# Performance work log

Hardware: AMD Instinct MI355X
Metric: run time of the kernel (lower is better)

Reference implementation:

```python
import jax, jax.numpy as jnp
import numpy as np

N_NODES = 100000
N_EDGES = 1600000
HIDDEN = 128
TOKENS = 50000
NUM_GRAPHS = 128


def _gru_cell(inp, h, Wih, Whh, bih, bhh):
    # PyTorch GRUCell math. Wih, Whh: [3H, H]; bih, bhh: [3H]
    gi = inp @ Wih.T + bih
    gh = h @ Whh.T + bhh
    i_r, i_z, i_n = jnp.split(gi, 3, axis=-1)
    h_r, h_z, h_n = jnp.split(gh, 3, axis=-1)
    r = jax.nn.sigmoid(i_r + h_r)
    z = jax.nn.sigmoid(i_z + h_z)
    n = jnp.tanh(i_n + r * h_n)
    return (1.0 - z) * n + z * h


def setup_inputs() -> dict:
    key = jax.random.key(0)
    ks = jax.random.split(key, 16)
    x = jax.random.randint(ks[0], (N_NODES,), 0, TOKENS)
    edge_index = jax.random.randint(ks[1], (2, N_EDGES), 0, N_NODES)
    batch = jnp.sort(jax.random.randint(ks[2], (N_NODES,), 0, NUM_GRAPHS))
    s = 0.05
    emb = jax.random.normal(ks[3], (TOKENS, HIDDEN), jnp.float32) * s
    Wih0 = jax.random.normal(ks[4], (3 * HIDDEN, HIDDEN), jnp.float32) * s
    Whh0 = jax.random.normal(ks[5], (3 * HIDDEN, HIDDEN), jnp.float32) * s
    bih0 = jnp.zeros((3 * HIDDEN,), jnp.float32)
    bhh0 = jnp.zeros((3 * HIDDEN,), jnp.float32)
    Wih1 = jax.random.normal(ks[6], (3 * HIDDEN, HIDDEN), jnp.float32) * s
    Whh1 = jax.random.normal(ks[7], (3 * HIDDEN, HIDDEN), jnp.float32) * s
    bih1 = jnp.zeros((3 * HIDDEN,), jnp.float32)
    bhh1 = jnp.zeros((3 * HIDDEN,), jnp.float32)
    dense_W = jax.random.normal(ks[8], (HIDDEN, HIDDEN), jnp.float32) * s
    dense_b = jnp.zeros((HIDDEN,), jnp.float32)
    clf_W = jax.random.normal(ks[9], (1, HIDDEN), jnp.float32) * s
    clf_b = jnp.zeros((1,), jnp.float32)
    return {"x": x, "edge_index": edge_index, "batch": batch, "emb": emb,
            "Wih0": Wih0, "Whh0": Whh0, "bih0": bih0, "bhh0": bhh0,
            "Wih1": Wih1, "Whh1": Whh1, "bih1": bih1, "bhh1": bhh1,
            "dense_W": dense_W, "dense_b": dense_b, "clf_W": clf_W, "clf_b": clf_b}


def reference(x, edge_index, batch, emb, Wih0, Whh0, bih0, bhh0,
              Wih1, Whh1, bih1, bhh1, dense_W, dense_b, clf_W, clf_b):
    src, dst = edge_index[0], edge_index[1]
    h = emb[x]  # [N, H]
    for (Wih, Whh, bih, bhh) in ((Wih0, Whh0, bih0, bhh0), (Wih1, Whh1, bih1, bhh1)):
        # gather source features, scatter-add into targets (aggr='add')
        agg = jax.ops.segment_sum(h[src], dst, num_segments=N_NODES)
        h = _gru_cell(agg, h, Wih, Whh, bih, bhh)
    # dropout is identity in eval mode
    h = h @ dense_W.T + dense_b
    g = jax.ops.segment_max(h, batch, num_segments=NUM_GRAPHS)  # global_max_pool
    out = jax.nn.sigmoid(g @ clf_W.T + clf_b)
    return out.squeeze(-1)  # [NUM_GRAPHS]
```

## Files before the change

### kernel.cpp

```cpp
#include <hip/hip_runtime.h>
#include <hip/hip_bf16.h>
#include <math.h>

#define HID 128
#define POOL_P 4
#define NPART 8
#define NCHUNK 32
#define MAXBIN 12544
#define FSLAB 520

typedef __attribute__((ext_vector_type(8))) short bf16x8;
typedef __attribute__((ext_vector_type(4))) float f32x4;
typedef __attribute__((ext_vector_type(4))) int int4v;

__device__ __forceinline__ short f2bf(float f) {
    unsigned int u = __float_as_uint(f);
    u += 0x7FFF + ((u >> 16) & 1);
    return (short)(u >> 16);
}
__device__ __forceinline__ float bf2f(short s) {
    return __uint_as_float(((unsigned int)(unsigned short)s) << 16);
}

__device__ __forceinline__ float fexp2(float x) {
    float r;
    asm("v_exp_f32 %0, %1\n\ts_nop 0" : "=v"(r) : "v"(x));
    return r;
}
__device__ __forceinline__ float frcp(float x) {
    float r;
    asm("v_rcp_f32 %0, %1\n\ts_nop 0" : "=v"(r) : "v"(x));
    return r;
}
__device__ __forceinline__ float fsigmoid(float x) {
    return frcp(1.f + fexp2(-1.44269504f * x));
}
__device__ __forceinline__ float ftanh(float x) {
    return 1.f - 2.f * frcp(1.f + fexp2(2.88539008f * x));
}

__global__ __launch_bounds__(1024) void radix_embed_k(const int* __restrict__ x,
                                                      const float* __restrict__ emb,
                                                      short* __restrict__ h, int nnodes,
                                                      const int* __restrict__ dst,
                                                      int* __restrict__ ghist,
                                                      int nedges, int NPB, int ECH) {
    __shared__ int lh[MAXBIN];
    const int t = threadIdx.x;
    if ((int)blockIdx.x < NPART * NCHUNK) {
        const int part = blockIdx.x & (NPART - 1);
        const int chunk = blockIdx.x >> 3;
        const int lo = part * NPB;
        const int hi = min(lo + NPB, nnodes);
        const int nb = hi - lo;
        for (int b = t; b < nb; b += 1024) lh[b] = 0;
        __syncthreads();
        const int e0 = chunk * ECH;
        const int e1 = min(nedges, e0 + ECH);
        for (int base = e0; base < e1; base += 4096) {
            int e = base + (t << 2);
            if (e + 4 <= e1) {
                int4v d4 = *(const int4v*)(dst + e);
                #pragma unroll
                for (int k = 0; k < 4; ++k) {
                    int d = d4[k];
                    if (d >= lo && d < hi) atomicAdd(&lh[d - lo], 1);
                }
            } else {
                for (int k = 0; k < 4 && e + k < e1; ++k) {
                    int d = dst[e + k];
                    if (d >= lo && d < hi) atomicAdd(&lh[d - lo], 1);
                }
            }
        }
        __syncthreads();
        int* out = ghist + (size_t)blockIdx.x * NPB;
        for (int b = t; b < nb; b += 1024) out[b] = lh[b];
    } else {
        int bi = blockIdx.x - NPART * NCHUNK;
        int tid = bi * 1024 + t;
        int node = tid >> 4;
        int c8 = tid & 15;
        if (node >= nnodes) return;
        int tok = x[node];
        float4 f0 = ((const float4*)emb)[(size_t)tok * 32 + c8 * 2];
        float4 f1 = ((const float4*)emb)[(size_t)tok * 32 + c8 * 2 + 1];
        bf16x8 o;
        o[0] = f2bf(f0.x); o[1] = f2bf(f0.y); o[2] = f2bf(f0.z); o[3] = f2bf(f0.w);
        o[4] = f2bf(f1.x); o[5] = f2bf(f1.y); o[6] = f2bf(f1.z); o[7] = f2bf(f1.w);
        *(bf16x8*)(h + (size_t)node * HID + c8 * 8) = o;
    }
}

__global__ __launch_bounds__(256) void chunksum_k(int* __restrict__ ghist,
                                                  int* __restrict__ degsum,
                                                  int nnodes, int NPB) {
    int node = blockIdx.x * 256 + threadIdx.x;
    if (node >= nnodes) return;
    int part = node / NPB;
    int bin = node - part * NPB;
    int running = 0;
    #pragma unroll 4
    for (int c = 0; c < NCHUNK; ++c) {
        size_t idx = (size_t)(part + NPART * c) * NPB + bin;
        int v = ghist[idx];
        ghist[idx] = running;
        running += v;
    }
    degsum[node] = running;
}

__global__ __launch_bounds__(1024) void scan_k(const int* __restrict__ deg,
                                               int* __restrict__ rowstart,
                                               int n, int* bsum, int* bflag, int nblocks) {
    __shared__ int wsum[16];
    __shared__ int prefix_s, total_s;
    const int b = blockIdx.x;
    const int t = threadIdx.x, lane = t & 63, w = t >> 6;
    const int i4 = b * 4096 + t * 4;
    int4 v = make_int4(0, 0, 0, 0);
    if (i4 + 3 < n) v = *(const int4*)(deg + i4);
    else if (i4 < n) {
        v.x = deg[i4];
        if (i4 + 1 < n) v.y = deg[i4 + 1];
        if (i4 + 2 < n) v.z = deg[i4 + 2];
    }
    int s1 = v.x + v.y, s2 = s1 + v.z, s3 = s2 + v.w;
    int sum = s3;
    #pragma unroll
    for (int off = 1; off < 64; off <<= 1) {
        int o = __shfl_up(sum, off, 64);
        if (lane >= off) sum += o;
    }
    if (lane == 63) wsum[w] = sum;
    __syncthreads();
    if (t == 0) {
        int run = 0;
        #pragma unroll
        for (int k = 0; k < 16; ++k) { int xx = wsum[k]; wsum[k] = run; run += xx; }
        total_s = run;
        atomicExch(&bsum[b], run);
        __threadfence();
        atomicExch(&bflag[b], 1);
    }
    __syncthreads();
    if (w == 0) {
        int p = 0;
        if (lane < b) {
            while (atomicAdd(&bflag[lane], 0) == 0) {}
            p = atomicAdd(&bsum[lane], 0);
        }
        #pragma unroll
        for (int off = 32; off >= 1; off >>= 1) p += __shfl_down(p, off, 64);
        if (lane == 0) prefix_s = p;
    }
    __syncthreads();
    const int excl = (sum - s3) + wsum[w] + prefix_s;
    if (i4 + 3 < n) {
        *(int4*)(rowstart + i4) = make_int4(excl, excl + v.x, excl + s1, excl + s2);
    } else if (i4 < n) {
        rowstart[i4] = excl;
        if (i4 + 1 < n) rowstart[i4 + 1] = excl + v.x;
        if (i4 + 2 < n) rowstart[i4 + 2] = excl + s1;
    }
    if (b == nblocks - 1 && t == 1023) rowstart[n] = prefix_s + total_s;
}

__global__ __launch_bounds__(1024) void fill2_k(const int* __restrict__ src,
                                                const int* __restrict__ dst,
                                                const int* __restrict__ rowstart,
                                                const int* __restrict__ ghist,
                                                int* __restrict__ sorted_src,
                                                int nedges, int nnodes, int NPB, int ECH) {
    __shared__ int cur[MAXBIN];
    const int t = threadIdx.x;
    const int part = blockIdx.x & (NPART - 1);
    const int chunk = blockIdx.x >> 3;
    const int lo = part * NPB;
    const int hi = min(lo + NPB, nnodes);
    const int nb = hi - lo;
    const int* base = ghist + (size_t)blockIdx.x * NPB;
    for (int b = t; b < nb; b += 1024)
        cur[b] = rowstart[lo + b] + base[b];
    __syncthreads();
    const int e0 = chunk * ECH;
    const int e1 = min(nedges, e0 + ECH);
    for (int bb = e0; bb < e1; bb += 4096) {
        int e = bb + (t << 2);
        if (e + 4 <= e1) {
            int4v d4 = *(const int4v*)(dst + e);
            #pragma unroll
            for (int k = 0; k < 4; ++k) {
                int d = d4[k];
                if (d >= lo && d < hi) {
                    int s = src[e + k];
                    int pos = atomicAdd(&cur[d - lo], 1);
                    sorted_src[pos] = s;
                }
            }
        } else {
            for (int k = 0; k < 4 && e + k < e1; ++k) {
                int d = dst[e + k];
                if (d >= lo && d < hi) {
                    int s = src[e + k];
                    int pos = atomicAdd(&cur[d - lo], 1);
                    sorted_src[pos] = s;
                }
            }
        }
    }
}

__global__ __launch_bounds__(256) void gather_k(const int* __restrict__ rowstart,
                                                const int* __restrict__ sorted_src,
                                                const short* __restrict__ h,
                                                short* __restrict__ agg, int nnodes) {
    int tid = blockIdx.x * 256 + threadIdx.x;
    int node = tid >> 4;
    int l = tid & 15;
    if (node >= nnodes) return;
    int beg = rowstart[node];
    int end = rowstart[node + 1];
    const bf16x8* hr = (const bf16x8*)h;
    float a[8];
    #pragma unroll
    for (int i = 0; i < 8; ++i) a[i] = 0.f;
    int e = beg;
    for (; e + 4 <= end; e += 4) {
        int s0 = sorted_src[e];
        int s1 = sorted_src[e + 1];
        int s2 = sorted_src[e + 2];
        int s3 = sorted_src[e + 3];
        bf16x8 v0 = hr[(size_t)s0 * 16 + l];
        bf16x8 v1 = hr[(size_t)s1 * 16 + l];
        bf16x8 v2 = hr[(size_t)s2 * 16 + l];
        bf16x8 v3 = hr[(size_t)s3 * 16 + l];
        #pragma unroll
        for (int i = 0; i < 8; ++i) a[i] += bf2f(v0[i]);
        #pragma unroll
        for (int i = 0; i < 8; ++i) a[i] += bf2f(v1[i]);
        #pragma unroll
        for (int i = 0; i < 8; ++i) a[i] += bf2f(v2[i]);
        #pragma unroll
        for (int i = 0; i < 8; ++i) a[i] += bf2f(v3[i]);
    }
    for (; e < end; ++e) {
        bf16x8 v0 = hr[(size_t)sorted_src[e] * 16 + l];
        #pragma unroll
        for (int i = 0; i < 8; ++i) a[i] += bf2f(v0[i]);
    }
    bf16x8 o;
    #pragma unroll
    for (int i = 0; i < 8; ++i) o[i] = f2bf(a[i]);
    *(bf16x8*)(agg + (size_t)node * HID + l * 8) = o;
}

__global__ __launch_bounds__(256) void pack_all_k(const float* __restrict__ Wih0,
                                                  const float* __restrict__ Whh0,
                                                  const float* __restrict__ Wih1,
                                                  const float* __restrict__ Whh1,
                                                  const float* __restrict__ dW,
                                                  short* __restrict__ P0,
                                                  short* __restrict__ P1,
                                                  short* __restrict__ Pd) {
    int b = blockIdx.x;
    const float* WA; const float* WB; short* P; int ntilesA; int tile;
    if (b < 48)      { WA = Wih0; WB = Whh0; P = P0; ntilesA = 24; tile = b; }
    else if (b < 96) { WA = Wih1; WB = Whh1; P = P1; ntilesA = 24; tile = b - 48; }
    else             { WA = dW;   WB = dW;   P = Pd; ntilesA = 8;  tile = b - 96; }
    const int t = threadIdx.x;
    const int lane = t & 63, k0 = t >> 6;
    const float* W;
    int row;
    if (tile < ntilesA) { W = WA; row = tile * 16 + (lane & 15); }
    else                { W = WB; row = (tile - ntilesA) * 16 + (lane & 15); }
    const int k = k0 * 32 + (lane >> 4) * 8;
    const float4 f0 = *(const float4*)(W + row * HID + k);
    const float4 f1 = *(const float4*)(W + row * HID + k + 4);
    short4 o0 = make_short4(f2bf(f0.x), f2bf(f0.y), f2bf(f0.z), f2bf(f0.w));
    short4 o1 = make_short4(f2bf(f1.x), f2bf(f1.y), f2bf(f1.z), f2bf(f1.w));
    short* dstp = P + ((size_t)(tile * 4 + k0) * 64 + lane) * 8;
    *(short4*)(dstp) = o0;
    *(short4*)(dstp + 4) = o1;
}


__global__ __launch_bounds__(256) void gru_mfma_k(const short* __restrict__ agg,
                                                  const short* __restrict__ hin,
                                                  short* __restrict__ hout,
                                                  const short* __restrict__ P,
                                                  const float* __restrict__ bih,
                                                  const float* __restrict__ bhh,
                                                  int nnodes) {
    __shared__ short As[4 * FSLAB];
    __shared__ short Hs[4 * FSLAB];
    const int t = threadIdx.x;
    const int mbase = blockIdx.x * 16;
    {
        int row = t >> 4, c8 = t & 15;
        int node = mbase + row;
        bf16x8 a = (bf16x8){0,0,0,0,0,0,0,0};
        bf16x8 hh = (bf16x8){0,0,0,0,0,0,0,0};
        if (node < nnodes) {
            a  = *(const bf16x8*)(agg + (size_t)node * HID + c8 * 8);
            hh = *(const bf16x8*)(hin + (size_t)node * HID + c8 * 8);
        }
        int off = (c8 >> 2) * FSLAB + ((c8 & 3) * 16 + row) * 8;
        *(bf16x8*)&As[off] = a;
        *(bf16x8*)&Hs[off] = hh;
    }
    __syncthreads();

    const int w = t >> 6, lane = t & 63;
    const int ml = lane & 15, kq = lane >> 4;
    const int j0 = w * 32;

    f32x4 acc[12];
    #pragma unroll
    for (int i = 0; i < 12; ++i) acc[i] = (f32x4){0.f, 0.f, 0.f, 0.f};

    const short* Pb = P + (size_t)lane * 8;

    #pragma unroll
    for (int k0 = 0; k0 < 4; ++k0) {
        bf16x8 aa = *(const bf16x8*)&As[k0 * FSLAB + lane * 8];
        bf16x8 ah = *(const bf16x8*)&Hs[k0 * FSLAB + lane * 8];
        #pragma unroll
        for (int m = 0; m < 2; ++m) {
            #pragma unroll
            for (int g = 0; g < 3; ++g) {
                #pragma unroll
                for (int ctt = 0; ctt < 2; ++ctt) {
                    const int tile = m * 24 + g * 8 + (w << 1) + ctt;
                    bf16x8 bb = *(const bf16x8*)(Pb + (size_t)(tile * 4 + k0) * 512);
                    const int idx = (m * 3 + g) * 2 + ctt;
                    acc[idx] = __builtin_amdgcn_mfma_f32_16x16x32_bf16(
                        (m == 0) ? aa : ah, bb, acc[idx], 0, 0, 0);
                }
            }
        }
    }

    #pragma unroll
    for (int ctt = 0; ctt < 2; ++ctt) {
        const int col = j0 + ctt * 16 + ml;
        const float b_ir = bih[col], b_iz = bih[col + 128], b_in = bih[col + 256];
        const float b_hr = bhh[col], b_hz = bhh[col + 128], b_hn = bhh[col + 256];
        const int hbase = w * FSLAB + (2 * ctt + (ml >> 3)) * 128 + (ml & 7);
        #pragma unroll
        for (int r = 0; r < 4; ++r) {
            const int row = kq * 4 + r;
            const int node = mbase + row;
            float ir = acc[0 + ctt][r] + b_ir;
            float iz = acc[2 + ctt][r] + b_iz;
            float in_ = acc[4 + ctt][r] + b_in;
            float hr = acc[6 + ctt][r] + b_hr;
            float hz = acc[8 + ctt][r] + b_hz;
            float hn = acc[10 + ctt][r] + b_hn;
            float rr = fsigmoid(ir + hr);
            float z  = fsigmoid(iz + hz);
            float n  = ftanh(in_ + rr * hn);
            if (node < nnodes) {
                float hval = bf2f(Hs[hbase + row * 8]);
                hout[(size_t)node * HID + col] = f2bf((1.f - z) * n + z * hval);
            }
        }
    }
}

__global__ __launch_bounds__(256) void gru_dense_k(const short* __restrict__ agg,
                                                   const short* __restrict__ hin,
                                                   short* __restrict__ yout,
                                                   const short* __restrict__ P,
                                                   const float* __restrict__ bih,
                                                   const float* __restrict__ bhh,
                                                   const short* __restrict__ Pd,
                                                   const float* __restrict__ db,
                                                   int nnodes) {
    __shared__ short As[4 * FSLAB];
    __shared__ short Hs[4 * FSLAB];
    const int t = threadIdx.x;
    const int mbase = blockIdx.x * 16;
    {
        int row = t >> 4, c8 = t & 15;
        int node = mbase + row;
        bf16x8 a = (bf16x8){0,0,0,0,0,0,0,0};
        bf16x8 hh = (bf16x8){0,0,0,0,0,0,0,0};
        if (node < nnodes) {
            a  = *(const bf16x8*)(agg + (size_t)node * HID + c8 * 8);
            hh = *(const bf16x8*)(hin + (size_t)node * HID + c8 * 8);
        }
        int off = (c8 >> 2) * FSLAB + ((c8 & 3) * 16 + row) * 8;
        *(bf16x8*)&As[off] = a;
        *(bf16x8*)&Hs[off] = hh;
    }
    __syncthreads();

    const int w = t >> 6, lane = t & 63;
    const int ml = lane & 15, kq = lane >> 4;
    const int j0 = w * 32;

    f32x4 acc[12];
    #pragma unroll
    for (int i = 0; i < 12; ++i) acc[i] = (f32x4){0.f, 0.f, 0.f, 0.f};

    const short* Pb = P + (size_t)lane * 8;

    #pragma unroll
    for (int k0 = 0; k0 < 4; ++k0) {
        bf16x8 aa = *(const bf16x8*)&As[k0 * FSLAB + lane * 8];
        bf16x8 ah = *(const bf16x8*)&Hs[k0 * FSLAB + lane * 8];
        #pragma unroll
        for (int m = 0; m < 2; ++m) {
            #pragma unroll
            for (int g = 0; g < 3; ++g) {
                #pragma unroll
                for (int ctt = 0; ctt < 2; ++ctt) {
                    const int tile = m * 24 + g * 8 + (w << 1) + ctt;
                    bf16x8 bb = *(const bf16x8*)(Pb + (size_t)(tile * 4 + k0) * 512);
                    const int idx = (m * 3 + g) * 2 + ctt;
                    acc[idx] = __builtin_amdgcn_mfma_f32_16x16x32_bf16(
                        (m == 0) ? aa : ah, bb, acc[idx], 0, 0, 0);
                }
            }
        }
    }

    short hnew[2][4];
    #pragma unroll
    for (int ctt = 0; ctt < 2; ++ctt) {
        const int col = j0 + ctt * 16 + ml;
        const float b_ir = bih[col], b_iz = bih[col + 128], b_in = bih[col + 256];
        const float b_hr = bhh[col], b_hz = bhh[col + 128], b_hn = bhh[col + 256];
        const int hbase = w * FSLAB + (2 * ctt + (ml >> 3)) * 128 + (ml & 7);
        #pragma unroll
        for (int r = 0; r < 4; ++r) {
            const int row = kq * 4 + r;
            float ir = acc[0 + ctt][r] + b_ir;
            float iz = acc[2 + ctt][r] + b_iz;
            float in_ = acc[4 + ctt][r] + b_in;
            float hr = acc[6 + ctt][r] + b_hr;
            float hz = acc[8 + ctt][r] + b_hz;
            float hn = acc[10 + ctt][r] + b_hn;
            float rr = fsigmoid(ir + hr);
            float z  = fsigmoid(iz + hz);
            float n  = ftanh(in_ + rr * hn);
            float hval = bf2f(Hs[hbase + row * 8]);
            hnew[ctt][r] = f2bf((1.f - z) * n + z * hval);
        }
    }

    __syncthreads();
    #pragma unroll
    for (int ctt = 0; ctt < 2; ++ctt) {
        const int hbase = w * FSLAB + (2 * ctt + (ml >> 3)) * 128 + (ml & 7);
        #pragma unroll
        for (int r = 0; r < 4; ++r)
            As[hbase + (kq * 4 + r) * 8] = hnew[ctt][r];
    }
    __syncthreads();

    f32x4 dacc[2];
    dacc[0] = (f32x4){0.f, 0.f, 0.f, 0.f};
    dacc[1] = (f32x4){0.f, 0.f, 0.f, 0.f};
    const short* Pbd = Pd + (size_t)lane * 8;
    #pragma unroll
    for (int k0 = 0; k0 < 4; ++k0) {
        bf16x8 aa = *(const bf16x8*)&As[k0 * FSLAB + lane * 8];
        #pragma unroll
        for (int ctt = 0; ctt < 2; ++ctt) {
            const int tile = (w << 1) + ctt;
            bf16x8 bb = *(const bf16x8*)(Pbd + (size_t)(tile * 4 + k0) * 512);
            dacc[ctt] = __builtin_amdgcn_mfma_f32_16x16x32_bf16(aa, bb, dacc[ctt], 0, 0, 0);
        }
    }
    #pragma unroll
    for (int ctt = 0; ctt < 2; ++ctt) {
        const int col = j0 + ctt * 16 + ml;
        const float bias = db[col];
        #pragma unroll
        for (int r = 0; r < 4; ++r) {
            const int node = mbase + kq * 4 + r;
            if (node < nnodes)
                yout[(size_t)node * HID + col] = f2bf(dacc[ctt][r] + bias);
        }
    }
}

__global__ __launch_bounds__(256) void pool_k(const short* __restrict__ xh,
                                              const int* __restrict__ batch,
                                              int nnodes, float* __restrict__ pmax) {
    const int g = blockIdx.x >> 2;
    const int p = blockIdx.x & (POOL_P - 1);
    int lo = 0, hi = nnodes;
    while (lo < hi) { int mid = (lo + hi) >> 1; if (batch[mid] < g) lo = mid + 1; else hi = mid; }
    int start = lo;
    lo = 0; hi = nnodes;
    while (lo < hi) { int mid = (lo + hi) >> 1; if (batch[mid] < g + 1) lo = mid + 1; else hi = mid; }
    int end = lo;
    int len = end - start;
    int q0 = start + (int)(((long long)len * p) / POOL_P);
    int q1 = start + (int)(((long long)len * (p + 1)) / POOL_P);

    const int rg = threadIdx.x >> 6;
    const int j2 = threadIdx.x & 63;
    float m0 = -INFINITY, m1 = -INFINITY;
    for (int i = q0 + rg; i < q1; i += 4) {
        unsigned int u = *(const unsigned int*)(xh + (size_t)i * HID + j2 * 2);
        m0 = fmaxf(m0, __uint_as_float(u << 16));
        m1 = fmaxf(m1, __uint_as_float(u & 0xFFFF0000u));
    }
    __shared__ float pm[4][130];
    pm[rg][j2 * 2] = m0;
    pm[rg][j2 * 2 + 1] = m1;
    __syncthreads();
    if (rg == 0) {
        float a = fmaxf(fmaxf(pm[0][j2 * 2], pm[1][j2 * 2]), fmaxf(pm[2][j2 * 2], pm[3][j2 * 2]));
        float c = fmaxf(fmaxf(pm[0][j2 * 2 + 1], pm[1][j2 * 2 + 1]), fmaxf(pm[2][j2 * 2 + 1], pm[3][j2 * 2 + 1]));
        *(float2*)(pmax + (size_t)blockIdx.x * HID + j2 * 2) = make_float2(a, c);
    }
}

__global__ __launch_bounds__(128) void clf_k(const float* __restrict__ pmax,
                                             const float* __restrict__ W,
                                             const float* __restrict__ b,
                                             float* __restrict__ out) {
    __shared__ float red[2];
    const int g = blockIdx.x;
    const int t = threadIdx.x;
    float m = -INFINITY;
    #pragma unroll
    for (int p = 0; p < POOL_P; ++p)
        m = fmaxf(m, pmax[((size_t)g * POOL_P + p) * HID + t]);
    float v = m * W[t];
    #pragma unroll
    for (int off = 32; off >= 1; off >>= 1) v += __shfl_down(v, off, 64);
    if ((t & 63) == 0) red[t >> 6] = v;
    __syncthreads();
    if (t == 0) {
        float s = red[0] + red[1] + b[0];
        out[g] = 1.f / (1.f + expf(-s));
    }
}

extern "C" void kernel_launch(void* const* d_in, const int* in_sizes, int n_in,
                              void* d_out, int out_size, void* d_ws, size_t ws_size,
                              hipStream_t stream) {
    const int* x      = (const int*)d_in[0];
    const int* ei     = (const int*)d_in[1];
    const int* batch  = (const int*)d_in[2];
    const float* emb  = (const float*)d_in[3];
    const float* Wih0 = (const float*)d_in[4];
    const float* Whh0 = (const float*)d_in[5];
    const float* bih0 = (const float*)d_in[6];
    const float* bhh0 = (const float*)d_in[7];
    const float* Wih1 = (const float*)d_in[8];
    const float* Whh1 = (const float*)d_in[9];
    const float* bih1 = (const float*)d_in[10];
    const float* bhh1 = (const float*)d_in[11];
    const float* dW   = (const float*)d_in[12];
    const float* db   = (const float*)d_in[13];
    const float* cW   = (const float*)d_in[14];
    const float* cb   = (const float*)d_in[15];

    const int N = in_sizes[0];
    const int E = in_sizes[1] / 2;
    const int NG = out_size;
    const size_t NH = (size_t)N * HID;
    const int NPB = (N + NPART - 1) / NPART;
    const int ECH = (E + NCHUNK - 1) / NCHUNK;

    short* hb0 = (short*)d_ws;
    short* hb1 = hb0 + NH;
    short* hb2 = hb1 + NH;
    short* P0  = hb2 + NH;
    short* P1  = P0 + 48 * 4 * 64 * 8;
    short* Pd  = P1 + 48 * 4 * 64 * 8;
    float* pmax = (float*)(Pd + 8 * 4 * 64 * 8);
    int* bflag      = (int*)(pmax + (size_t)NG * POOL_P * HID);
    int* bsum       = bflag + 64;
    int* degsum     = bsum + 64;
    int* rowstart   = degsum + N;
    int* ghist      = rowstart + (N + 4);
    int* sorted_src = ghist + (size_t)NPART * NCHUNK * NPB;

    const int* esrc = ei;
    const int* edst = ei + E;

    dim3 blk(256);
    int embGrid256  = (N * 16 + 255) / 256;
    int embGrid1024 = (N * 16 + 1023) / 1024;
    int tileGrid = (N + 15) / 16;
    const int scanBlocks = (N + 4095) / 4096;

    pack_all_k<<<104, blk, 0, stream>>>(Wih0, Whh0, Wih1, Whh1, dW, P0, P1, Pd);

    hipMemsetAsync(bflag, 0, 64 * sizeof(int), stream);
    radix_embed_k<<<NPART * NCHUNK + embGrid1024, dim3(1024), 0, stream>>>(
        x, emb, hb0, N, edst, ghist, E, NPB, ECH);

    chunksum_k<<<(N + 255) / 256, blk, 0, stream>>>(ghist, degsum, N, NPB);
    scan_k<<<scanBlocks, dim3(1024), 0, stream>>>(degsum, rowstart, N, bsum, bflag, scanBlocks);
    fill2_k<<<NPART * NCHUNK, dim3(1024), 0, stream>>>(esrc, edst, rowstart, ghist, sorted_src,
                                                       E, N, NPB, ECH);

    gather_k<<<embGrid256, blk, 0, stream>>>(rowstart, sorted_src, hb0, hb1, N);
    gru_mfma_k<<<tileGrid, blk, 0, stream>>>(hb1, hb0, hb2, P0, bih0, bhh0, N);

    gather_k<<<embGrid256, blk, 0, stream>>>(rowstart, sorted_src, hb2, hb1, N);
    gru_dense_k<<<tileGrid, blk, 0, stream>>>(hb1, hb2, hb0, P1, bih1, bhh1, Pd, db, N);

    pool_k<<<NG * POOL_P, blk, 0, stream>>>(hb0, batch, N, pmax);
    clf_k<<<NG, dim3(128), 0, stream>>>(pmax, cW, cb, (float*)d_out);
}
```

Baseline: 440.0 us.

## Use persistent GRU/dense kernels with register-resident weights and double-buffered tiles

Replaces the one-block-per-16-node GRU kernels with a persistent grid of 768 blocks. Each block holds its slice of packed weight fragments in registers, covering half the output columns, and loops over row tiles while prefetching the next tile's agg and h rows into a second LDS buffer. The fused GRU+dense kernel is split into a second gru_rl_k plus a separate persistent dense kernel. This removes repeated weight reloads per tile and overlaps global loads with MFMA work. The cost is higher register pressure, each tile's inputs being read by two column-half blocks, and an extra write and read of the layer-2 hidden state.

```diff
diff --git a/kernel.cpp b/kernel.cpp
--- a/kernel.cpp
+++ b/kernel.cpp
@@ -285,205 +285,169 @@
 }
 
 
-__global__ __launch_bounds__(256) void gru_mfma_k(const short* __restrict__ agg,
-                                                  const short* __restrict__ hin,
-                                                  short* __restrict__ hout,
-                                                  const short* __restrict__ P,
-                                                  const float* __restrict__ bih,
-                                                  const float* __restrict__ bhh,
-                                                  int nnodes) {
-    __shared__ short As[4 * FSLAB];
-    __shared__ short Hs[4 * FSLAB];
+__global__ __launch_bounds__(256) void gru_rl_k(const short* __restrict__ agg,
+                                                const short* __restrict__ hin,
+                                                short* __restrict__ hout,
+                                                const short* __restrict__ P,
+                                                const float* __restrict__ bih,
+                                                const float* __restrict__ bhh,
+                                                int nnodes, int ntiles) {
+    __shared__ short As[2][4 * FSLAB];
+    __shared__ short Hs[2][4 * FSLAB];
     const int t = threadIdx.x;
-    const int mbase = blockIdx.x * 16;
+    const int lane = t & 63, w = t >> 6;
+    const int ch = blockIdx.x & 1;
+    const int cw = ch * 4 + w;
+    const int ml = lane & 15, kq = lane >> 4;
+    const int col = cw * 16 + ml;
+
+    const float b_ir = bih[col], b_iz = bih[col + 128], b_in = bih[col + 256];
+    const float b_hr = bhh[col], b_hz = bhh[col + 128], b_hn = bhh[col + 256];
+
+    bf16x8 B[2][3][4];
+    #pragma unroll
+    for (int m = 0; m < 2; ++m)
+        #pragma unroll
+        for (int g = 0; g < 3; ++g)
+            #pragma unroll
+            for (int k0 = 0; k0 < 4; ++k0)
+                B[m][g][k0] = *(const bf16x8*)(P +
+                    ((size_t)((m * 24 + g * 8 + cw) * 4 + k0) * 64 + lane) * 8);
+
+    const int srow = t >> 4, sc8 = t & 15;
+    const int soff = (sc8 >> 2) * FSLAB + (srow * 4 + (sc8 & 3)) * 8;
+    const int roff = (ml * 4 + kq) * 8;
+    const int hoff = (col >> 5) * FSLAB + ((col >> 3) & 3) * 8 + (col & 7);
+
+    const int rt0 = blockIdx.x >> 1;
+    const int stride = gridDim.x >> 1;
+
     {
-        int row = t >> 4, c8 = t & 15;
-        int node = mbase + row;
-        bf16x8 a = (bf16x8){0,0,0,0,0,0,0,0};
-        bf16x8 hh = (bf16x8){0,0,0,0,0,0,0,0};
+        int node = rt0 * 16 + srow;
+        bf16x8 a = (bf16x8){0,0,0,0,0,0,0,0}, hh = a;
         if (node < nnodes) {
-            a  = *(const bf16x8*)(agg + (size_t)node * HID + c8 * 8);
-            hh = *(const bf16x8*)(hin + (size_t)node * HID + c8 * 8);
-        }
-        int off = (c8 >> 2) * FSLAB + ((c8 & 3) * 16 + row) * 8;
-        *(bf16x8*)&As[off] = a;
-        *(bf16x8*)&Hs[off] = hh;
-    }
-    __syncthreads();
-
-    const int w = t >> 6, lane = t & 63;
-    const int ml = lane & 15, kq = lane >> 4;
-    const int j0 = w * 32;
-
-    f32x4 acc[12];
-    #pragma unroll
-    for (int i = 0; i < 12; ++i) acc[i] = (f32x4){0.f, 0.f, 0.f, 0.f};
-
-    const short* Pb = P + (size_t)lane * 8;
-
-    #pragma unroll
-    for (int k0 = 0; k0 < 4; ++k0) {
-        bf16x8 aa = *(const bf16x8*)&As[k0 * FSLAB + lane * 8];
-        bf16x8 ah = *(const bf16x8*)&Hs[k0 * FSLAB + lane * 8];
-        #pragma unroll
-        for (int m = 0; m < 2; ++m) {
+            a  = *(const bf16x8*)(agg + (size_t)node * HID + sc8 * 8);
+            hh = *(const bf16x8*)(hin + (size_t)node * HID + sc8 * 8);
+        }
+        *(bf16x8*)&As[0][soff] = a;
+        *(bf16x8*)&Hs[0][soff] = hh;
+    }
+    __syncthreads();
+
+    int buf = 0;
+    for (int rt = rt0; rt < ntiles; rt += stride, buf ^= 1) {
+        const int nrt = rt + stride;
+        bf16x8 pa = (bf16x8){0,0,0,0,0,0,0,0}, ph = pa;
+        if (nrt < ntiles) {
+            int node = nrt * 16 + srow;
+            if (node < nnodes) {
+                pa = *(const bf16x8*)(agg + (size_t)node * HID + sc8 * 8);
+                ph = *(const bf16x8*)(hin + (size_t)node * HID + sc8 * 8);
+            }
+        }
+
+        f32x4 acc[6];
+        #pragma unroll
+        for (int i = 0; i < 6; ++i) acc[i] = (f32x4){0.f, 0.f, 0.f, 0.f};
+        #pragma unroll
+        for (int k0 = 0; k0 < 4; ++k0) {
+            bf16x8 aa = *(const bf16x8*)&As[buf][k0 * FSLAB + roff];
+            bf16x8 ah = *(const bf16x8*)&Hs[buf][k0 * FSLAB + roff];
             #pragma unroll
             for (int g = 0; g < 3; ++g) {
-                #pragma unroll
-                for (int ctt = 0; ctt < 2; ++ctt) {
-                    const int tile = m * 24 + g * 8 + (w << 1) + ctt;
-                    bf16x8 bb = *(const bf16x8*)(Pb + (size_t)(tile * 4 + k0) * 512);
-                    const int idx = (m * 3 + g) * 2 + ctt;
-                    acc[idx] = __builtin_amdgcn_mfma_f32_16x16x32_bf16(
-                        (m == 0) ? aa : ah, bb, acc[idx], 0, 0, 0);
-                }
+                acc[g]     = __builtin_amdgcn_mfma_f32_16x16x32_bf16(aa, B[0][g][k0], acc[g], 0, 0, 0);
+                acc[3 + g] = __builtin_amdgcn_mfma_f32_16x16x32_bf16(ah, B[1][g][k0], acc[3 + g], 0, 0, 0);
             }
         }
-    }
-
-    #pragma unroll
-    for (int ctt = 0; ctt < 2; ++ctt) {
-        const int col = j0 + ctt * 16 + ml;
-        const float b_ir = bih[col], b_iz = bih[col + 128], b_in = bih[col + 256];
-        const float b_hr = bhh[col], b_hz = bhh[col + 128], b_hn = bhh[col + 256];
-        const int hbase = w * FSLAB + (2 * ctt + (ml >> 3)) * 128 + (ml & 7);
+
+        const int mbase = rt * 16;
         #pragma unroll
         for (int r = 0; r < 4; ++r) {
             const int row = kq * 4 + r;
             const int node = mbase + row;
-            float ir = acc[0 + ctt][r] + b_ir;
-            float iz = acc[2 + ctt][r] + b_iz;
-            float in_ = acc[4 + ctt][r] + b_in;
-            float hr = acc[6 + ctt][r] + b_hr;
-            float hz = acc[8 + ctt][r] + b_hz;
-            float hn = acc[10 + ctt][r] + b_hn;
+            float ir = acc[0][r] + b_ir;
+            float iz = acc[1][r] + b_iz;
+            float in_ = acc[2][r] + b_in;
+            float hr = acc[3][r] + b_hr;
+            float hz = acc[4][r] + b_hz;
+            float hn = acc[5][r] + b_hn;
             float rr = fsigmoid(ir + hr);
             float z  = fsigmoid(iz + hz);
             float n  = ftanh(in_ + rr * hn);
             if (node < nnodes) {
-                float hval = bf2f(Hs[hbase + row * 8]);
+                float hval = bf2f(Hs[buf][hoff + row * 32]);
                 hout[(size_t)node * HID + col] = f2bf((1.f - z) * n + z * hval);
             }
         }
-    }
-}
-
-__global__ __launch_bounds__(256) void gru_dense_k(const short* __restrict__ agg,
-                                                   const short* __restrict__ hin,
-                                                   short* __restrict__ yout,
-                                                   const short* __restrict__ P,
-                                                   const float* __restrict__ bih,
-                                                   const float* __restrict__ bhh,
-                                                   const short* __restrict__ Pd,
-                                                   const float* __restrict__ db,
-                                                   int nnodes) {
-    __shared__ short As[4 * FSLAB];
-    __shared__ short Hs[4 * FSLAB];
+
+        if (nrt < ntiles) {
+            *(bf16x8*)&As[buf ^ 1][soff] = pa;
+            *(bf16x8*)&Hs[buf ^ 1][soff] = ph;
+        }
+        __syncthreads();
+    }
+}
+
+__global__ __launch_bounds__(256) void dense_rl_k(const short* __restrict__ x,
+                                                  short* __restrict__ y,
+                                                  const short* __restrict__ Pd,
+                                                  const float* __restrict__ db,
+                                                  int nnodes, int ntiles) {
+    __shared__ short Xs[2][4 * FSLAB];
     const int t = threadIdx.x;
-    const int mbase = blockIdx.x * 16;
+    const int lane = t & 63, w = t >> 6;
+    const int ch = blockIdx.x & 1;
+    const int cw = ch * 4 + w;
+    const int ml = lane & 15, kq = lane >> 4;
+    const int col = cw * 16 + ml;
+    const float bias = db[col];
+
+    bf16x8 B[4];
+    #pragma unroll
+    for (int k0 = 0; k0 < 4; ++k0)
+        B[k0] = *(const bf16x8*)(Pd + ((size_t)(cw * 4 + k0) * 64 + lane) * 8);
+
+    const int srow = t >> 4, sc8 = t & 15;
+    const int soff = (sc8 >> 2) * FSLAB + (srow * 4 + (sc8 & 3)) * 8;
+    const int roff = (ml * 4 + kq) * 8;
+
+    const int rt0 = blockIdx.x >> 1;
+    const int stride = gridDim.x >> 1;
+
     {
-        int row = t >> 4, c8 = t & 15;
-        int node = mbase + row;
-        bf16x8 a = (bf16x8){0,0,0,0,0,0,0,0};
-        bf16x8 hh = (bf16x8){0,0,0,0,0,0,0,0};
-        if (node < nnodes) {
-            a  = *(const bf16x8*)(agg + (size_t)node * HID + c8 * 8);
-            hh = *(const bf16x8*)(hin + (size_t)node * HID + c8 * 8);
-        }
-        int off = (c8 >> 2) * FSLAB + ((c8 & 3) * 16 + row) * 8;
-        *(bf16x8*)&As[off] = a;
-        *(bf16x8*)&Hs[off] = hh;
-    }
-    __syncthreads();
-
-    const int w = t >> 6, lane = t & 63;
-    const int ml = lane & 15, kq = lane >> 4;
-    const int j0 = w * 32;
-
-    f32x4 acc[12];
-    #pragma unroll
-    for (int i = 0; i < 12; ++i) acc[i] = (f32x4){0.f, 0.f, 0.f, 0.f};
-
-    const short* Pb = P + (size_t)lane * 8;
-
-    #pragma unroll
-    for (int k0 = 0; k0 < 4; ++k0) {
-        bf16x8 aa = *(const bf16x8*)&As[k0 * FSLAB + lane * 8];
-        bf16x8 ah = *(const bf16x8*)&Hs[k0 * FSLAB + lane * 8];
-        #pragma unroll
-        for (int m = 0; m < 2; ++m) {
-            #pragma unroll
-            for (int g = 0; g < 3; ++g) {
-                #pragma unroll
-                for (int ctt = 0; ctt < 2; ++ctt) {
-                    const int tile = m * 24 + g * 8 + (w << 1) + ctt;
-                    bf16x8 bb = *(const bf16x8*)(Pb + (size_t)(tile * 4 + k0) * 512);
-                    const int idx = (m * 3 + g) * 2 + ctt;
-                    acc[idx] = __builtin_amdgcn_mfma_f32_16x16x32_bf16(
-                        (m == 0) ? aa : ah, bb, acc[idx], 0, 0, 0);
-                }
-            }
-        }
-    }
-
-    short hnew[2][4];
-    #pragma unroll
-    for (int ctt = 0; ctt < 2; ++ctt) {
-        const int col = j0 + ctt * 16 + ml;
-        const float b_ir = bih[col], b_iz = bih[col + 128], b_in = bih[col + 256];
-        const float b_hr = bhh[col], b_hz = bhh[col + 128], b_hn = bhh[col + 256];
-        const int hbase = w * FSLAB + (2 * ctt + (ml >> 3)) * 128 + (ml & 7);
-        #pragma unroll
-        for (int r = 0; r < 4; ++r) {
-            const int row = kq * 4 + r;
-            float ir = acc[0 + ctt][r] + b_ir;
-            float iz = acc[2 + ctt][r] + b_iz;
-            float in_ = acc[4 + ctt][r] + b_in;
-            float hr = acc[6 + ctt][r] + b_hr;
-            float hz = acc[8 + ctt][r] + b_hz;
-            float hn = acc[10 + ctt][r] + b_hn;
-            float rr = fsigmoid(ir + hr);
-            float z  = fsigmoid(iz + hz);
-            float n  = ftanh(in_ + rr * hn);
-            float hval = bf2f(Hs[hbase + row * 8]);
-            hnew[ctt][r] = f2bf((1.f - z) * n + z * hval);
-        }
-    }
-
-    __syncthreads();
-    #pragma unroll
-    for (int ctt = 0; ctt < 2; ++ctt) {
-        const int hbase = w * FSLAB + (2 * ctt + (ml >> 3)) * 128 + (ml & 7);
-        #pragma unroll
-        for (int r = 0; r < 4; ++r)
-            As[hbase + (kq * 4 + r) * 8] = hnew[ctt][r];
-    }
-    __syncthreads();
-
-    f32x4 dacc[2];
-    dacc[0] = (f32x4){0.f, 0.f, 0.f, 0.f};
-    dacc[1] = (f32x4){0.f, 0.f, 0.f, 0.f};
-    const short* Pbd = Pd + (size_t)lane * 8;
-    #pragma unroll
-    for (int k0 = 0; k0 < 4; ++k0) {
-        bf16x8 aa = *(const bf16x8*)&As[k0 * FSLAB + lane * 8];
-        #pragma unroll
-        for (int ctt = 0; ctt < 2; ++ctt) {
-            const int tile = (w << 1) + ctt;
-            bf16x8 bb = *(const bf16x8*)(Pbd + (size_t)(tile * 4 + k0) * 512);
-            dacc[ctt] = __builtin_amdgcn_mfma_f32_16x16x32_bf16(aa, bb, dacc[ctt], 0, 0, 0);
-        }
-    }
-    #pragma unroll
-    for (int ctt = 0; ctt < 2; ++ctt) {
-        const int col = j0 + ctt * 16 + ml;
-        const float bias = db[col];
+        int node = rt0 * 16 + srow;
+        bf16x8 xv = (bf16x8){0,0,0,0,0,0,0,0};
+        if (node < nnodes) xv = *(const bf16x8*)(x + (size_t)node * HID + sc8 * 8);
+        *(bf16x8*)&Xs[0][soff] = xv;
+    }
+    __syncthreads();
+
+    int buf = 0;
+    for (int rt = rt0; rt < ntiles; rt += stride, buf ^= 1) {
+        const int nrt = rt + stride;
+        bf16x8 px = (bf16x8){0,0,0,0,0,0,0,0};
+        if (nrt < ntiles) {
+            int node = nrt * 16 + srow;
+            if (node < nnodes) px = *(const bf16x8*)(x + (size_t)node * HID + sc8 * 8);
+        }
+
+        f32x4 acc = (f32x4){0.f, 0.f, 0.f, 0.f};
+        #pragma unroll
+        for (int k0 = 0; k0 < 4; ++k0) {
+            bf16x8 aa = *(const bf16x8*)&Xs[buf][k0 * FSLAB + roff];
+            acc = __builtin_amdgcn_mfma_f32_16x16x32_bf16(aa, B[k0], acc, 0, 0, 0);
+        }
+
+        const int mbase = rt * 16;
         #pragma unroll
         for (int r = 0; r < 4; ++r) {
             const int node = mbase + kq * 4 + r;
             if (node < nnodes)
-                yout[(size_t)node * HID + col] = f2bf(dacc[ctt][r] + bias);
-        }
+                y[(size_t)node * HID + col] = f2bf(acc[r] + bias);
+        }
+
+        if (nrt < ntiles) *(bf16x8*)&Xs[buf ^ 1][soff] = px;
+        __syncthreads();
     }
 }
 
@@ -590,8 +554,9 @@
     dim3 blk(256);
     int embGrid256  = (N * 16 + 255) / 256;
     int embGrid1024 = (N * 16 + 1023) / 1024;
-    int tileGrid = (N + 15) / 16;
+    int ntiles = (N + 15) / 16;
     const int scanBlocks = (N + 4095) / 4096;
+    const int NB = 768;
 
     pack_all_k<<<104, blk, 0, stream>>>(Wih0, Whh0, Wih1, Whh1, dW, P0, P1, Pd);
 
@@ -605,11 +570,13 @@
                                                        E, N, NPB, ECH);
 
     gather_k<<<embGrid256, blk, 0, stream>>>(rowstart, sorted_src, hb0, hb1, N);
-    gru_mfma_k<<<tileGrid, blk, 0, stream>>>(hb1, hb0, hb2, P0, bih0, bhh0, N);
+    gru_rl_k<<<NB, blk, 0, stream>>>(hb1, hb0, hb2, P0, bih0, bhh0, N, ntiles);
 
     gather_k<<<embGrid256, blk, 0, stream>>>(rowstart, sorted_src, hb2, hb1, N);
-    gru_dense_k<<<tileGrid, blk, 0, stream>>>(hb1, hb2, hb0, P1, bih1, bhh1, Pd, db, N);
-
-    pool_k<<<NG * POOL_P, blk, 0, stream>>>(hb0, batch, N, pmax);
+    gru_rl_k<<<NB, blk, 0, stream>>>(hb1, hb2, hb0, P1, bih1, bhh1, N, ntiles);
+
+    dense_rl_k<<<NB, blk, 0, stream>>>(hb0, hb2, Pd, db, N, ntiles);
+
+    pool_k<<<NG * POOL_P, blk, 0, stream>>>(hb2, batch, N, pmax);
     clf_k<<<NG, dim3(128), 0, stream>>>(pmax, cW, cb, (float*)d_out);
 }
```

New measurement: 399.6 us. 1.1x faster.
